# Kernel tuning notes

Hardware: AMD Instinct MI355X
Metric: run time of the kernel (lower is better)

Reference implementation:

```python
import jax, jax.numpy as jnp
import numpy as np

DIM = 192
NH = 4
B, H, W = 4, 128, 128


def _conv1x1(x, w, b):
    # x: [b,c,h,w], w: [o,c], b: [o]
    return jnp.einsum('oc,bchw->bohw', w, x) + b[None, :, None, None]


def _dwconv3(x, w, b):
    # depthwise 3x3, w: [C,1,3,3]
    y = jax.lax.conv_general_dilated(
        x, w, window_strides=(1, 1), padding='SAME',
        feature_group_count=x.shape[1],
        dimension_numbers=('NCHW', 'OIHW', 'NCHW'))
    return y + b[None, :, None, None]


def _to_heads(x, nh):
    b, c, h, w = x.shape
    return x.reshape(b, nh, c // nh, h * w)  # b head c (hw)


def _l2norm(x):
    # torch F.normalize(dim=-1): x / max(||x||, eps)
    n = jnp.sqrt(jnp.sum(x * x, axis=-1, keepdims=True))
    return x / jnp.maximum(n, 1e-12)


def _chan_attn(q, k, v, temp):
    # q,k,v: [b,head,c,n]; temp: [head,1,1] -> broadcasts over [b,head,c,c]
    scores = jnp.einsum('bhcn,bhdn->bhcd', q, k) * temp
    a = jax.nn.softmax(scores, axis=-1)
    return jnp.einsum('bhcd,bhdn->bhcn', a, v)


def setup_inputs() -> dict:
    key = jax.random.key(0)
    ks = jax.random.split(key, 16)
    d3 = 3 * DIM
    inp = {
        'sar': jax.random.normal(ks[0], (B, DIM, H, W), jnp.float32),
        'ms': jax.random.normal(ks[1], (B, DIM, H, W), jnp.float32),
        'ms_qkv_w': jax.random.normal(ks[2], (d3, DIM), jnp.float32) * 0.02,
        'ms_qkv_b': jnp.zeros((d3,), jnp.float32),
        'ms_dw_w': jax.random.normal(ks[3], (d3, 1, 3, 3), jnp.float32) * 0.1,
        'ms_dw_b': jnp.zeros((d3,), jnp.float32),
        'ms_temp': jnp.ones((NH, 1, 1), jnp.float32),
        'sar_qkv_w': jax.random.normal(ks[4], (d3, DIM), jnp.float32) * 0.02,
        'sar_qkv_b': jnp.zeros((d3,), jnp.float32),
        'sar_dw_w': jax.random.normal(ks[5], (d3, 1, 3, 3), jnp.float32) * 0.1,
        'sar_dw_b': jnp.zeros((d3,), jnp.float32),
        'sar_temp': jnp.ones((NH, 1, 1), jnp.float32),
        'ms_proj_w': jax.random.normal(ks[6], (DIM, 2 * DIM), jnp.float32) * 0.02,
        'ms_proj_b': jnp.zeros((DIM,), jnp.float32),
        'sar_proj_w': jax.random.normal(ks[7], (DIM, DIM), jnp.float32) * 0.02,
        'sar_proj_b': jnp.zeros((DIM,), jnp.float32),
    }
    return inp


def reference(sar, ms, ms_qkv_w, ms_qkv_b, ms_dw_w, ms_dw_b, ms_temp,
              sar_qkv_w, sar_qkv_b, sar_dw_w, sar_dw_b, sar_temp,
              ms_proj_w, ms_proj_b, sar_proj_w, sar_proj_b):
    b, c, h, w = ms.shape

    ms_qkv = _dwconv3(_conv1x1(ms, ms_qkv_w, ms_qkv_b), ms_dw_w, ms_dw_b)
    ms_q, ms_k, ms_v = jnp.split(ms_qkv, 3, axis=1)
    ms_q = _l2norm(_to_heads(ms_q, NH))
    ms_k = _l2norm(_to_heads(ms_k, NH))
    ms_v = _to_heads(ms_v, NH)

    sar_qkv = _dwconv3(_conv1x1(sar, sar_qkv_w, sar_qkv_b), sar_dw_w, sar_dw_b)
    sar_q, sar_k, sar_v = jnp.split(sar_qkv, 3, axis=1)
    sar_q = _l2norm(_to_heads(sar_q, NH))
    sar_k = _l2norm(_to_heads(sar_k, NH))
    sar_v = _to_heads(sar_v, NH)

    ms_self = _chan_attn(ms_q, ms_k, ms_v, ms_temp).reshape(b, c, h, w)
    sar_self = _chan_attn(sar_q, sar_k, sar_v, sar_temp).reshape(b, c, h, w)
    cross = _chan_attn(sar_q, ms_k, sar_v, ms_temp).reshape(b, c, h, w)

    sar_out = sar + _conv1x1(sar_self, sar_proj_w, sar_proj_b)
    ms_cat = jnp.concatenate([ms_self, cross + ms_self], axis=1)
    ms_out = ms + _conv1x1(ms_cat, ms_proj_w, ms_proj_b)
    return (sar_out, ms_out)
```

## Files before the change

kernel.cpp:

```cpp
#include <hip/hip_runtime.h>
#include <hip/hip_bf16.h>
#include <cstdint>

#define DIMC 192
#define BB 4
#define NN 16384
#define D3 576
#define CHD 48
#define WWID 128
#define HHGT 128
#define NCK 64
#define CKW 256

typedef short short8 __attribute__((ext_vector_type(8)));
typedef float f32x4 __attribute__((ext_vector_type(4)));

union FragU { uint4 u4; short8 s8; };

__device__ __forceinline__ float bf2f(uint16_t v) {
    return __uint_as_float(((uint32_t)v) << 16);
}
__device__ __forceinline__ float2 upk2(uint32_t u) {
    float2 r;
    r.x = __uint_as_float(u << 16);
    r.y = __uint_as_float(u & 0xffff0000u);
    return r;
}
__device__ __forceinline__ uint16_t f2bf(float f) {
    uint32_t x = __float_as_uint(f);
    return (uint16_t)((x + 0x7fffu + ((x >> 16) & 1u)) >> 16);
}
__device__ __forceinline__ uint4 pack8(const uint16_t* v) {
    uint4 u;
    u.x = (uint32_t)v[0] | ((uint32_t)v[1] << 16);
    u.y = (uint32_t)v[2] | ((uint32_t)v[3] << 16);
    u.z = (uint32_t)v[4] | ((uint32_t)v[5] << 16);
    u.w = (uint32_t)v[6] | ((uint32_t)v[7] << 16);
    return u;
}

__global__ __launch_bounds__(256) void k_prep(
    const float* __restrict__ w0, const float* __restrict__ w1,
    const float* __restrict__ w2, const float* __restrict__ w3,
    uint16_t* __restrict__ o0, uint16_t* __restrict__ o1,
    uint16_t* __restrict__ o2a, uint16_t* __restrict__ o2b,
    uint16_t* __restrict__ o3)
{
    int i = blockIdx.x * 256 + threadIdx.x;
    if (i < 110592) { o0[i] = f2bf(w0[i]); return; }
    i -= 110592;
    if (i < 110592) { o1[i] = f2bf(w1[i]); return; }
    i -= 110592;
    if (i < 36864) {
        const int o = i / DIMC, c = i % DIMC;
        o2a[i] = f2bf(w2[o * 384 + c] + w2[o * 384 + DIMC + c]);
        o2b[i] = f2bf(w2[o * 384 + DIMC + c]);
        return;
    }
    i -= 36864;
    if (i < 36864) o3[i] = f2bf(w3[i]);
}

__global__ __launch_bounds__(512, 4) void k_conv_both(
    const float* __restrict__ ms, const float* __restrict__ sarp,
    const uint16_t* __restrict__ w_ms, const uint16_t* __restrict__ w_sar,
    const float* __restrict__ b_ms, const float* __restrict__ b_sar,
    uint16_t* __restrict__ out_ms, uint16_t* __restrict__ out_sar)
{
    __shared__ uint16_t xs[128][200];
    __shared__ uint16_t wstA[64][200];
    const int t = threadIdx.x;
    const int bid = blockIdx.x;
    const int path = bid >> 9;
    const int rem = bid & 511;
    const int nb = rem & 127, b = rem >> 7;
    const int n0 = nb * 128;

    const float* x        = path ? sarp  : ms;
    const uint16_t* wsrc  = path ? w_sar : w_ms;
    const float* bias     = path ? b_sar : b_ms;
    uint16_t* out         = path ? out_sar : out_ms;

    const int lane = t & 63, wvid = t >> 6;
    const int lm = lane & 15, g = lane >> 4;
    const int wm = wvid >> 2, wn = wvid & 3;
    const int wm_ = t >> 3, wq = t & 7;

    {
        const int sn = t & 127, kq = t >> 7;
        const int sg = (sn >> 3) & 3;
        const float* xcol = x + ((size_t)b * DIMC + kq * 48) * NN + n0 + sn;
        for (int u = 0; u < 6; ++u) {
            uint16_t vals[8];
#pragma unroll
            for (int j = 0; j < 8; ++j)
                vals[j] = f2bf(xcol[(size_t)(u * 8 + j) * NN]);
            *(uint4*)&xs[sn][((kq * 6 + u) ^ sg) * 8] = pack8(vals);
        }
    }
    {
        const uint16_t* wrow = wsrc + (size_t)wm_ * DIMC;
#pragma unroll
        for (int i = 0; i < 3; ++i) {
            const int unit = i * 8 + wq;
            *(uint4*)&wstA[wm_][(unit ^ (wm_ & 7)) * 8] = *(const uint4*)&wrow[unit * 8];
        }
    }
    __syncthreads();

    FragU bfr[6][2];
#pragma unroll
    for (int ks = 0; ks < 6; ++ks)
#pragma unroll
        for (int nj = 0; nj < 2; ++nj) {
            const int row = wn * 32 + nj * 16 + lm;
            bfr[ks][nj].u4 = *(const uint4*)&xs[row][((ks * 4 + g) ^ ((row >> 3) & 3)) * 8];
        }
    __syncthreads();

    uint16_t* xsf  = &xs[0][0];
    uint16_t* wstB = xsf;
    uint16_t* sw   = xsf + 12800 + wvid * 1280;

    for (int mb = 0; mb < 9; ++mb) {
        const uint16_t* cur = (mb & 1) ? wstB : &wstA[0][0];
        uint16_t* nxt       = (mb & 1) ? &wstA[0][0] : wstB;
        uint4 wreg[3];
        if (mb < 8) {
            const uint16_t* wrow = wsrc + (size_t)((mb + 1) * 64 + wm_) * DIMC;
#pragma unroll
            for (int i = 0; i < 3; ++i)
                wreg[i] = *(const uint4*)&wrow[(i * 8 + wq) * 8];
        }
        f32x4 acc[2][2];
#pragma unroll
        for (int mi = 0; mi < 2; ++mi)
#pragma unroll
            for (int nj = 0; nj < 2; ++nj) acc[mi][nj] = (f32x4){0.f, 0.f, 0.f, 0.f};
#pragma unroll
        for (int ks = 0; ks < 6; ++ks) {
            FragU afr[2];
#pragma unroll
            for (int mi = 0; mi < 2; ++mi) {
                const int row = wm * 32 + mi * 16 + lm;
                afr[mi].u4 = *(const uint4*)&cur[row * 200 + ((ks * 4 + g) ^ (row & 7)) * 8];
            }
#pragma unroll
            for (int mi = 0; mi < 2; ++mi)
#pragma unroll
                for (int nj = 0; nj < 2; ++nj)
                    acc[mi][nj] = __builtin_amdgcn_mfma_f32_16x16x32_bf16(
                        afr[mi].s8, bfr[ks][nj].s8, acc[mi][nj], 0, 0, 0);
        }
        if (mb < 8) {
#pragma unroll
            for (int i = 0; i < 3; ++i) {
                const int unit = i * 8 + wq;
                *(uint4*)&nxt[wm_ * 200 + ((unit ^ (wm_ & 7))) * 8] = wreg[i];
            }
        }
#pragma unroll
        for (int mi = 0; mi < 2; ++mi) {
            const int rbase = mb * 64 + wm * 32 + mi * 16 + g * 4;
            const float4 bv = *(const float4*)&bias[rbase];
            const float bva[4] = {bv.x, bv.y, bv.z, bv.w};
#pragma unroll
            for (int nj = 0; nj < 2; ++nj)
#pragma unroll
                for (int r = 0; r < 4; ++r)
                    sw[(mi * 16 + g * 4 + r) * 40 + nj * 16 + lm] =
                        f2bf(acc[mi][nj][r] + bva[r]);
        }
        {
            const int row2 = lane >> 1, q = lane & 1;
            uint4 v0 = *(const uint4*)&sw[row2 * 40 + q * 16];
            uint4 v1 = *(const uint4*)&sw[row2 * 40 + q * 16 + 8];
            const int grow = mb * 64 + wm * 32 + row2;
            uint16_t* ob = &out[((size_t)b * D3 + grow) * NN + n0 + wn * 32 + q * 16];
            *(uint4*)ob       = v0;
            *(uint4*)(ob + 8) = v1;
        }
        __syncthreads();
    }
}

__global__ __launch_bounds__(512, 4) void k_proj_both(
    const uint16_t* __restrict__ sar_self, const uint16_t* __restrict__ ms_self,
    const uint16_t* __restrict__ crossb,
    const uint16_t* __restrict__ wp_sar, const uint16_t* __restrict__ wp1_ms,
    const uint16_t* __restrict__ wp2_ms,
    const float* __restrict__ b_sar, const float* __restrict__ b_ms,
    const float* __restrict__ resid_sar, const float* __restrict__ resid_ms,
    float* __restrict__ out_sar, float* __restrict__ out_ms)
{
    __shared__ uint16_t xs[128][200];
    __shared__ uint16_t wstA[64][200];
    const int t = threadIdx.x;
    const int bid = blockIdx.x;
    const int path = bid >> 9;
    const int rem = bid & 511;
    const int nb = rem & 127, b = rem >> 7;
    const int n0 = nb * 128;
    const int nph = path ? 2 : 1;

    const float* bias  = path ? b_ms : b_sar;
    const float* resid = path ? resid_ms : resid_sar;
    float* out         = path ? out_ms : out_sar;

    const int lane = t & 63, wvid = t >> 6;
    const int lm = lane & 15, g = lane >> 4;
    const int wm = wvid >> 2, wn = wvid & 3;
    const int wm_ = t >> 3, wq = t & 7;

    uint16_t* xsf  = &xs[0][0];
    uint16_t* wstB = xsf;

    f32x4 acc[3][2][2];
#pragma unroll
    for (int mb = 0; mb < 3; ++mb)
#pragma unroll
        for (int mi = 0; mi < 2; ++mi)
#pragma unroll
            for (int nj = 0; nj < 2; ++nj) acc[mb][mi][nj] = (f32x4){0.f, 0.f, 0.f, 0.f};

    for (int ph = 0; ph < nph; ++ph) {
        const uint16_t* xsrc = path ? (ph ? crossb : ms_self) : sar_self;
        const uint16_t* wsrc = path ? (ph ? wp2_ms : wp1_ms) : wp_sar;
        {
            const int p = t & 63, kg = t >> 6;
            const int sg = (p >> 2) & 3;
            const uint16_t* xcol = xsrc + ((size_t)b * DIMC + kg * 24) * NN + n0 + p * 2;
            for (int chn = 0; chn < 3; ++chn) {
                uint32_t v[8];
#pragma unroll
                for (int j = 0; j < 8; ++j)
                    v[j] = *(const uint32_t*)&xcol[(size_t)(chn * 8 + j) * NN];
                uint4 lo4, hi4;
                lo4.x = (v[0] & 0xffffu) | (v[1] << 16);
                lo4.y = (v[2] & 0xffffu) | (v[3] << 16);
                lo4.z = (v[4] & 0xffffu) | (v[5] << 16);
                lo4.w = (v[6] & 0xffffu) | (v[7] << 16);
                hi4.x = (v[0] >> 16) | (v[1] & 0xffff0000u);
                hi4.y = (v[2] >> 16) | (v[3] & 0xffff0000u);
                hi4.z = (v[4] >> 16) | (v[5] & 0xffff0000u);
                hi4.w = (v[6] >> 16) | (v[7] & 0xffff0000u);
                const int unit = (kg * 3 + chn) ^ sg;
                *(uint4*)&xs[p * 2][unit * 8]     = lo4;
                *(uint4*)&xs[p * 2 + 1][unit * 8] = hi4;
            }
        }
        {
            const uint16_t* wrow = wsrc + (size_t)wm_ * DIMC;
#pragma unroll
            for (int i = 0; i < 3; ++i) {
                const int unit = i * 8 + wq;
                *(uint4*)&wstA[wm_][(unit ^ (wm_ & 7)) * 8] = *(const uint4*)&wrow[unit * 8];
            }
        }
        __syncthreads();
        FragU bfr[6][2];
#pragma unroll
        for (int ks = 0; ks < 6; ++ks)
#pragma unroll
            for (int nj = 0; nj < 2; ++nj) {
                const int row = wn * 32 + nj * 16 + lm;
                bfr[ks][nj].u4 = *(const uint4*)&xs[row][((ks * 4 + g) ^ ((row >> 3) & 3)) * 8];
            }
        __syncthreads();

        for (int mb = 0; mb < 3; ++mb) {
            const uint16_t* cur = (mb & 1) ? wstB : &wstA[0][0];
            uint16_t* nxt       = (mb & 1) ? &wstA[0][0] : wstB;
            uint4 wreg[3];
            if (mb < 2) {
                const uint16_t* wrow = wsrc + (size_t)((mb + 1) * 64 + wm_) * DIMC;
#pragma unroll
                for (int i = 0; i < 3; ++i)
                    wreg[i] = *(const uint4*)&wrow[(i * 8 + wq) * 8];
            }
#pragma unroll
            for (int ks = 0; ks < 6; ++ks) {
                FragU afr[2];
#pragma unroll
                for (int mi = 0; mi < 2; ++mi) {
                    const int row = wm * 32 + mi * 16 + lm;
                    afr[mi].u4 = *(const uint4*)&cur[row * 200 + ((ks * 4 + g) ^ (row & 7)) * 8];
                }
#pragma unroll
                for (int mi = 0; mi < 2; ++mi)
#pragma unroll
                    for (int nj = 0; nj < 2; ++nj)
                        acc[mb][mi][nj] = __builtin_amdgcn_mfma_f32_16x16x32_bf16(
                            afr[mi].s8, bfr[ks][nj].s8, acc[mb][mi][nj], 0, 0, 0);
            }
            if (mb < 2) {
#pragma unroll
                for (int i = 0; i < 3; ++i) {
                    const int unit = i * 8 + wq;
                    *(uint4*)&nxt[wm_ * 200 + ((unit ^ (wm_ & 7))) * 8] = wreg[i];
                }
            }
            __syncthreads();
        }
    }
#pragma unroll
    for (int mb = 0; mb < 3; ++mb)
#pragma unroll
        for (int mi = 0; mi < 2; ++mi) {
            const int rbase = mb * 64 + wm * 32 + mi * 16 + g * 4;
            const float4 bv = *(const float4*)&bias[rbase];
            const float bva[4] = {bv.x, bv.y, bv.z, bv.w};
#pragma unroll
            for (int nj = 0; nj < 2; ++nj) {
                const int gcol = n0 + wn * 32 + nj * 16 + lm;
#pragma unroll
                for (int r = 0; r < 4; ++r) {
                    const size_t idx = ((size_t)b * DIMC + rbase + r) * NN + gcol;
                    out[idx] = resid[idx] + acc[mb][mi][nj][r] + bva[r];
                }
            }
        }
}

__global__ __launch_bounds__(256) void k_dw_both(
    const uint16_t* __restrict__ in0, const uint16_t* __restrict__ in1,
    const float* __restrict__ w_ms, const float* __restrict__ w_sar,
    const float* __restrict__ b_ms, const float* __restrict__ b_sar,
    uint16_t* __restrict__ out0, uint16_t* __restrict__ out1)
{
    __shared__ uint16_t lds[34 * 136];
    const int t = threadIdx.x;
    const int bid = blockIdx.x;
    const int yb = bid & 3;
    int bc = bid >> 2;
    const int path = (bc >= BB * D3);
    if (path) bc -= BB * D3;
    const int ch = bc % D3;
    const uint16_t* in = path ? in1 : in0;
    const float* w9    = path ? w_sar : w_ms;
    const float* bias  = path ? b_sar : b_ms;
    uint16_t* out      = path ? out1 : out0;

    const int y0 = yb * 32;
    const uint16_t* p = in + (size_t)bc * NN;

#pragma unroll
    for (int it = 0; it < 3; ++it) {
        const int u = it * 256 + t;
        if (u < 34 * 16) {
            const int r = u >> 4, seg = u & 15;
            const int gy = y0 - 1 + r;
            uint4 v = (gy >= 0 && gy < HHGT)
                ? *(const uint4*)(p + gy * WWID + seg * 8)
                : (uint4){0u, 0u, 0u, 0u};
            *(uint4*)&lds[r * 136 + seg * 8] = v;
        }
    }
    float wv[9];
#pragma unroll
    for (int k = 0; k < 9; ++k) wv[k] = w9[ch * 9 + k];
    const float base = bias[ch];
    __syncthreads();

    const int lr = t >> 3;
    const int x0 = (t & 7) * 16;
    float rv[3][18];
#pragma unroll
    for (int dy = 0; dy < 3; ++dy) {
        const uint16_t* lp = &lds[(lr + dy) * 136 + x0];
        uint4 a = *(const uint4*)lp;
        uint4 bq = *(const uint4*)(lp + 8);
        const uint16_t* av = (const uint16_t*)&a;
        const uint16_t* bv2 = (const uint16_t*)&bq;
#pragma unroll
        for (int j = 0; j < 8; ++j) {
            rv[dy][1 + j] = bf2f(av[j]);
            rv[dy][9 + j] = bf2f(bv2[j]);
        }
        rv[dy][0]  = (x0 > 0) ? bf2f(lds[(lr + dy) * 136 + x0 - 1]) : 0.f;
        rv[dy][17] = (x0 + 16 < WWID) ? bf2f(lds[(lr + dy) * 136 + x0 + 16]) : 0.f;
    }
    uint16_t ov[16];
#pragma unroll
    for (int j = 0; j < 16; ++j) {
        float a = base;
#pragma unroll
        for (int dy = 0; dy < 3; ++dy)
            a = fmaf(rv[dy][j], wv[dy * 3],
                fmaf(rv[dy][j + 1], wv[dy * 3 + 1],
                fmaf(rv[dy][j + 2], wv[dy * 3 + 2], a)));
        ov[j] = f2bf(a);
    }
    uint16_t* ob = out + (size_t)bc * NN + (y0 + lr) * WWID + x0;
    *(uint4*)ob       = pack8(&ov[0]);
    *(uint4*)(ob + 8) = pack8(&ov[8]);
}

__global__ __launch_bounds__(256) void k_scores_mfma(
    const uint16_t* __restrict__ qkv_ms, const uint16_t* __restrict__ qkv_sar,
    float* __restrict__ partial, float* __restrict__ sumsq)
{
    const int t = threadIdx.x;
    const int bid = blockIdx.x;
    const int ck = bid & (NCK - 1);
    const int pid = bid / NCK;
    const int h = pid & 3, b = pid >> 2;
    const int n0 = ck * CKW;
    const int lane = t & 63, w = t >> 6;

    const uint16_t* qm  = qkv_ms  + ((size_t)b * D3 + h * CHD) * NN;
    const uint16_t* km  = qkv_ms  + ((size_t)b * D3 + DIMC + h * CHD) * NN;
    const uint16_t* qsr = qkv_sar + ((size_t)b * D3 + h * CHD) * NN;
    const uint16_t* ksr = qkv_sar + ((size_t)b * D3 + DIMC + h * CHD) * NN;

    if (w < 3) {
        const uint16_t* qb = (w == 0) ? qm : qsr;
        const uint16_t* kb = (w == 1) ? ksr : km;
        const int lm = lane & 15, g = lane >> 4;
        f32x4 acc[3][3];
#pragma unroll
        for (int i = 0; i < 3; ++i)
#pragma unroll
            for (int j = 0; j < 3; ++j) acc[i][j] = (f32x4){0.f, 0.f, 0.f, 0.f};
#pragma unroll 2
        for (int kk = 0; kk < CKW / 32; ++kk) {
            const int nb2 = n0 + kk * 32 + g * 8;
            FragU qf[3], kf[3];
#pragma unroll
            for (int i = 0; i < 3; ++i)
                qf[i].u4 = *(const uint4*)&qb[(size_t)(i * 16 + lm) * NN + nb2];
#pragma unroll
            for (int j = 0; j < 3; ++j)
                kf[j].u4 = *(const uint4*)&kb[(size_t)(j * 16 + lm) * NN + nb2];
#pragma unroll
            for (int i = 0; i < 3; ++i)
#pragma unroll
                for (int j = 0; j < 3; ++j)
                    acc[i][j] = __builtin_amdgcn_mfma_f32_16x16x32_bf16(
                        qf[i].s8, kf[j].s8, acc[i][j], 0, 0, 0);
        }
        float* pd = partial + (((size_t)pid * 3 + w) * NCK + ck) * 2304;
        const int g4 = g * 4;
#pragma unroll
        for (int i = 0; i < 3; ++i)
#pragma unroll
            for (int j = 0; j < 3; ++j)
#pragma unroll
                for (int r = 0; r < 4; ++r)
                    pd[(i * 16 + g4 + r) * 48 + j * 16 + lm] = acc[i][j][r];
    } else {
#pragma unroll
        for (int rep = 0; rep < 3; ++rep) {
            const int rid = rep * 64 + lane;
            const int s = rid / CHD, c = rid % CHD;
            const uint16_t* rowp =
                (s == 0) ? qm  + (size_t)c * NN :
                (s == 1) ? km  + (size_t)c * NN :
                (s == 2) ? qsr + (size_t)c * NN :
                           ksr + (size_t)c * NN;
            float sum = 0.f;
#pragma unroll 4
            for (int u = 0; u < CKW / 8; ++u) {
                uint4 v = *(const uint4*)&rowp[n0 + u * 8];
                uint32_t uu[4] = {v.x, v.y, v.z, v.w};
#pragma unroll
                for (int q = 0; q < 4; ++q) {
                    float2 f = upk2(uu[q]);
                    sum = fmaf(f.x, f.x, fmaf(f.y, f.y, sum));
                }
            }
            sumsq[(((size_t)pid * NCK + ck) * 4 + s) * CHD + c] = sum;
        }
    }
}

__global__ __launch_bounds__(64) void k_softmax(
    const float* __restrict__ partial, const float* __restrict__ sumsq,
    const float* __restrict__ ms_temp, const float* __restrict__ sar_temp,
    float* __restrict__ A)
{
    const int lane = threadIdx.x;
    const int bi = blockIdx.x;
    const int c = bi % 48;
    const int pid = bi / 48;
    const int h = pid & 3, b = (pid >> 2) & 3, type = pid >> 4;
    const int pid16 = b * 4 + h;
    float s;
    if (lane < 48) {
        float accv = 0.f;
        const float* pp = partial + ((size_t)pid16 * 3 + type) * NCK * 2304 + c * 48 + lane;
#pragma unroll 8
        for (int ck = 0; ck < NCK; ++ck) accv += pp[(size_t)ck * 2304];
        const int qset = (type == 0) ? 0 : 2;
        const int kset = (type == 1) ? 3 : 1;
        float qsum = 0.f, ksum = 0.f;
        const float* sq = sumsq + (size_t)pid16 * NCK * 4 * CHD;
#pragma unroll 8
        for (int ck = 0; ck < NCK; ++ck) {
            qsum += sq[ck * 4 * CHD + qset * CHD + c];
            ksum += sq[ck * 4 * CHD + kset * CHD + lane];
        }
        const float tval = (type == 1) ? sar_temp[h] : ms_temp[h];
        const float qsc = 1.0f / fmaxf(sqrtf(qsum), 1e-12f);
        const float ksc = 1.0f / fmaxf(sqrtf(ksum), 1e-12f);
        s = accv * qsc * ksc * tval;
    } else {
        s = -3.0e38f;
    }
    float m = s;
#pragma unroll
    for (int o = 32; o > 0; o >>= 1) m = fmaxf(m, __shfl_xor(m, o));
    float e = (lane < 48) ? __expf(s - m) : 0.f;
    float sum = e;
#pragma unroll
    for (int o = 32; o > 0; o >>= 1) sum += __shfl_xor(sum, o);
    if (lane < 48) A[(size_t)pid * 2304 + c * 48 + lane] = e / sum;
}

__global__ __launch_bounds__(256) void k_apply_mfma(
    const float* __restrict__ A, const uint16_t* __restrict__ qkv_ms,
    const uint16_t* __restrict__ qkv_sar, uint16_t* __restrict__ attn)
{
    __shared__ uint16_t vs[256][40];
    __shared__ uint16_t as[48][40];
    __shared__ uint16_t sw_all[4][48][72];
    const int t = threadIdx.x;
    const int nb = blockIdx.x & 63;
    const int pid = blockIdx.x >> 6;
    const int h = pid & 3, b = (pid >> 2) & 3, type = pid >> 4;
    const int n0 = nb * 256;
    const uint16_t* vsrc = (type == 0) ? qkv_ms : qkv_sar;
    const uint16_t* vb = vsrc + ((size_t)b * D3 + 2 * DIMC + (size_t)h * CHD) * NN;
    const float* Ap = A + (size_t)pid * 2304;

    const int lane = t & 63, wvid = t >> 6;
    const int lm = lane & 15, g = lane >> 4;

    f32x4 acc[3][4];
#pragma unroll
    for (int i = 0; i < 3; ++i)
#pragma unroll
        for (int j = 0; j < 4; ++j) acc[i][j] = (f32x4){0.f, 0.f, 0.f, 0.f};

    for (int k0 = 0; k0 < 64; k0 += 32) {
        __syncthreads();
#pragma unroll
        for (int kh = 0; kh < 2; ++kh) {
            uint16_t vals[16];
#pragma unroll
            for (int j = 0; j < 16; ++j) {
                const int d = k0 + kh * 16 + j;
                vals[j] = (d < CHD) ? vb[(size_t)d * NN + n0 + t] : (uint16_t)0;
            }
            const int u0 = (2 * kh) ^ ((t >> 3) & 3);
            const int u1 = (2 * kh + 1) ^ ((t >> 3) & 3);
            *(uint4*)&vs[t][u0 * 8] = pack8(&vals[0]);
            *(uint4*)&vs[t][u1 * 8] = pack8(&vals[8]);
        }
        if (t < 192) {
            const int c = t >> 2, dq = t & 3;
            uint16_t av[8];
#pragma unroll
            for (int i = 0; i < 8; ++i) {
                const int d = k0 + dq * 8 + i;
                av[i] = (d < CHD) ? f2bf(Ap[c * CHD + d]) : (uint16_t)0;
            }
            const int u = dq ^ ((c >> 3) & 3);
            *(uint4*)&as[c][u * 8] = pack8(av);
        }
        __syncthreads();
        FragU afr[3], bfr[4];
#pragma unroll
        for (int mi = 0; mi < 3; ++mi) {
            const int row = mi * 16 + lm;
            afr[mi].u4 = *(const uint4*)&as[row][(g ^ ((row >> 3) & 3)) * 8];
        }
#pragma unroll
        for (int nj = 0; nj < 4; ++nj) {
            const int row = wvid * 64 + nj * 16 + lm;
            bfr[nj].u4 = *(const uint4*)&vs[row][(g ^ ((row >> 3) & 3)) * 8];
        }
#pragma unroll
        for (int mi = 0; mi < 3; ++mi)
#pragma unroll
            for (int nj = 0; nj < 4; ++nj)
                acc[mi][nj] = __builtin_amdgcn_mfma_f32_16x16x32_bf16(
                    afr[mi].s8, bfr[nj].s8, acc[mi][nj], 0, 0, 0);
    }

    uint16_t* ob = attn + (size_t)type * BB * DIMC * NN +
                   ((size_t)b * DIMC + (size_t)h * CHD) * NN;
    uint16_t* sw = &sw_all[wvid][0][0];
#pragma unroll
    for (int mi = 0; mi < 3; ++mi)
#pragma unroll
        for (int nj = 0; nj < 4; ++nj)
#pragma unroll
            for (int r = 0; r < 4; ++r)
                sw[(mi * 16 + g * 4 + r) * 72 + nj * 16 + lm] = f2bf(acc[mi][nj][r]);
    const int l8 = lane & 7, r8 = lane >> 3;
#pragma unroll
    for (int pass = 0; pass < 6; ++pass) {
        const int rr = pass * 8 + r8;
        uint4 v = *(const uint4*)&sw[rr * 72 + l8 * 8];
        *(uint4*)&ob[(size_t)rr * NN + n0 + wvid * 64 + l8 * 8] = v;
    }
}

extern "C" void kernel_launch(void* const* d_in, const int* in_sizes, int n_in,
                              void* d_out, int out_size, void* d_ws, size_t ws_size,
                              hipStream_t stream)
{
    const float* sar        = (const float*)d_in[0];
    const float* ms         = (const float*)d_in[1];
    const float* ms_qkv_w   = (const float*)d_in[2];
    const float* ms_qkv_b   = (const float*)d_in[3];
    const float* ms_dw_w    = (const float*)d_in[4];
    const float* ms_dw_b    = (const float*)d_in[5];
    const float* ms_temp    = (const float*)d_in[6];
    const float* sar_qkv_w  = (const float*)d_in[7];
    const float* sar_qkv_b  = (const float*)d_in[8];
    const float* sar_dw_w   = (const float*)d_in[9];
    const float* sar_dw_b   = (const float*)d_in[10];
    const float* sar_temp   = (const float*)d_in[11];
    const float* ms_proj_w  = (const float*)d_in[12];
    const float* ms_proj_b  = (const float*)d_in[13];
    const float* sar_proj_w = (const float*)d_in[14];
    const float* sar_proj_b = (const float*)d_in[15];

    char* ws = (char*)d_ws;
    uint16_t* tmp     = (uint16_t*)(ws);
    uint16_t* tmp2    = (uint16_t*)(d_out);
    uint16_t* qkv_ms  = (uint16_t*)(ws + 75497472ull);
    uint16_t* qkv_sar = (uint16_t*)(ws + 150994944ull);
    float* partial    = (float*)(ws);
    float* sumsq      = (float*)(ws + 33554432ull);
    float* Amat       = (float*)(ws + 230043648ull);
    uint16_t* wq_ms   = (uint16_t*)(ws + 230486016ull);
    uint16_t* wq_sar  = (uint16_t*)(ws + 230707200ull);
    uint16_t* wp1_ms  = (uint16_t*)(ws + 230928384ull);
    uint16_t* wp2_ms  = (uint16_t*)(ws + 231002112ull);
    uint16_t* wp_sar  = (uint16_t*)(ws + 231075840ull);
    uint16_t* attn    = tmp;

    float* out_sar = (float*)d_out;
    float* out_ms  = out_sar + (size_t)BB * DIMC * NN;

    dim3 b256(256);
    k_prep<<<dim3(1152), b256, 0, stream>>>(ms_qkv_w, sar_qkv_w, ms_proj_w, sar_proj_w,
                                            wq_ms, wq_sar, wp1_ms, wp2_ms, wp_sar);
    k_conv_both<<<dim3(1024), dim3(512), 0, stream>>>(
        ms, sar, wq_ms, wq_sar, ms_qkv_b, sar_qkv_b, tmp, tmp2);
    k_dw_both<<<dim3(2 * BB * D3 * 4), b256, 0, stream>>>(
        tmp, tmp2, ms_dw_w, sar_dw_w, ms_dw_b, sar_dw_b, qkv_ms, qkv_sar);

    k_scores_mfma<<<dim3(16 * NCK), b256, 0, stream>>>(qkv_ms, qkv_sar, partial, sumsq);
    k_softmax<<<dim3(48 * 48), dim3(64), 0, stream>>>(partial, sumsq, ms_temp, sar_temp, Amat);
    k_apply_mfma<<<dim3(48 * 64), b256, 0, stream>>>(Amat, qkv_ms, qkv_sar, attn);

    uint16_t* ms_self  = attn;
    uint16_t* sar_self = attn + (size_t)BB * DIMC * NN;
    uint16_t* crossb   = attn + 2ull * BB * DIMC * NN;
    k_proj_both<<<dim3(1024), dim3(512), 0, stream>>>(
        sar_self, ms_self, crossb, wp_sar, wp1_ms, wp2_ms,
        sar_proj_b, ms_proj_b, sar, ms, out_sar, out_ms);
}
```

Before: 324.4 us.

## Halve pixel tile and block size in 1x1 conv and projection kernels

The qkv conv and output projection kernels now process 64-pixel tiles with 256-thread blocks instead of 128-pixel tiles with 512 threads, doubling the grid to 2048 blocks. The LDS XOR swizzles are removed in favour of plain row-major indexing, and in the conv kernel the double-buffered weight staging becomes a single buffer reloaded after an extra barrier. The aim is more, smaller blocks with less shared memory each, for better occupancy and load balance. The cost is more redundant weight loads per pixel, possible LDS bank conflicts without the swizzle, and an added sync per weight tile.

```diff
diff --git a/kernel.cpp b/kernel.cpp
--- a/kernel.cpp
+++ b/kernel.cpp
@@ -61,20 +61,20 @@
     if (i < 36864) o3[i] = f2bf(w3[i]);
 }
 
-__global__ __launch_bounds__(512, 4) void k_conv_both(
+__global__ __launch_bounds__(256, 3) void k_conv_both(
     const float* __restrict__ ms, const float* __restrict__ sarp,
     const uint16_t* __restrict__ w_ms, const uint16_t* __restrict__ w_sar,
     const float* __restrict__ b_ms, const float* __restrict__ b_sar,
     uint16_t* __restrict__ out_ms, uint16_t* __restrict__ out_sar)
 {
-    __shared__ uint16_t xs[128][200];
-    __shared__ uint16_t wstA[64][200];
+    __shared__ uint16_t xs[64][200];
+    __shared__ uint16_t wst[64][200];
     const int t = threadIdx.x;
     const int bid = blockIdx.x;
-    const int path = bid >> 9;
-    const int rem = bid & 511;
-    const int nb = rem & 127, b = rem >> 7;
-    const int n0 = nb * 128;
+    const int path = bid >> 10;
+    const int rem = bid & 1023;
+    const int nb = rem & 255, b = rem >> 8;
+    const int n0 = nb * 64;
 
     const float* x        = path ? sarp  : ms;
     const uint16_t* wsrc  = path ? w_sar : w_ms;
@@ -83,27 +83,26 @@
 
     const int lane = t & 63, wvid = t >> 6;
     const int lm = lane & 15, g = lane >> 4;
-    const int wm = wvid >> 2, wn = wvid & 3;
-    const int wm_ = t >> 3, wq = t & 7;
+    const int wm = wvid >> 1, wn = wvid & 1;
+    const int wm_ = t >> 2, wq = t & 3;
 
     {
-        const int sn = t & 127, kq = t >> 7;
-        const int sg = (sn >> 3) & 3;
-        const float* xcol = x + ((size_t)b * DIMC + kq * 48) * NN + n0 + sn;
+        const int sn = t & 63, kh = t >> 6;
+        const float* xcol = x + ((size_t)b * DIMC + kh * 48) * NN + n0 + sn;
         for (int u = 0; u < 6; ++u) {
             uint16_t vals[8];
 #pragma unroll
             for (int j = 0; j < 8; ++j)
                 vals[j] = f2bf(xcol[(size_t)(u * 8 + j) * NN]);
-            *(uint4*)&xs[sn][((kq * 6 + u) ^ sg) * 8] = pack8(vals);
+            *(uint4*)&xs[sn][(kh * 6 + u) * 8] = pack8(vals);
         }
     }
     {
         const uint16_t* wrow = wsrc + (size_t)wm_ * DIMC;
 #pragma unroll
-        for (int i = 0; i < 3; ++i) {
-            const int unit = i * 8 + wq;
-            *(uint4*)&wstA[wm_][(unit ^ (wm_ & 7)) * 8] = *(const uint4*)&wrow[unit * 8];
+        for (int i = 0; i < 6; ++i) {
+            const int unit = i * 4 + wq;
+            *(uint4*)&wst[wm_][unit * 8] = *(const uint4*)&wrow[unit * 8];
         }
     }
     __syncthreads();
@@ -114,23 +113,19 @@
 #pragma unroll
         for (int nj = 0; nj < 2; ++nj) {
             const int row = wn * 32 + nj * 16 + lm;
-            bfr[ks][nj].u4 = *(const uint4*)&xs[row][((ks * 4 + g) ^ ((row >> 3) & 3)) * 8];
+            bfr[ks][nj].u4 = *(const uint4*)&xs[row][ks * 32 + g * 8];
         }
     __syncthreads();
 
-    uint16_t* xsf  = &xs[0][0];
-    uint16_t* wstB = xsf;
-    uint16_t* sw   = xsf + 12800 + wvid * 1280;
+    uint16_t* sw = &xs[0][0] + wvid * 1280;
 
     for (int mb = 0; mb < 9; ++mb) {
-        const uint16_t* cur = (mb & 1) ? wstB : &wstA[0][0];
-        uint16_t* nxt       = (mb & 1) ? &wstA[0][0] : wstB;
-        uint4 wreg[3];
+        uint4 wreg[6];
         if (mb < 8) {
             const uint16_t* wrow = wsrc + (size_t)((mb + 1) * 64 + wm_) * DIMC;
 #pragma unroll
-            for (int i = 0; i < 3; ++i)
-                wreg[i] = *(const uint4*)&wrow[(i * 8 + wq) * 8];
+            for (int i = 0; i < 6; ++i)
+                wreg[i] = *(const uint4*)&wrow[(i * 4 + wq) * 8];
         }
         f32x4 acc[2][2];
 #pragma unroll
@@ -143,7 +138,7 @@
 #pragma unroll
             for (int mi = 0; mi < 2; ++mi) {
                 const int row = wm * 32 + mi * 16 + lm;
-                afr[mi].u4 = *(const uint4*)&cur[row * 200 + ((ks * 4 + g) ^ (row & 7)) * 8];
+                afr[mi].u4 = *(const uint4*)&wst[row][ks * 32 + g * 8];
             }
 #pragma unroll
             for (int mi = 0; mi < 2; ++mi)
@@ -151,13 +146,6 @@
                 for (int nj = 0; nj < 2; ++nj)
                     acc[mi][nj] = __builtin_amdgcn_mfma_f32_16x16x32_bf16(
                         afr[mi].s8, bfr[ks][nj].s8, acc[mi][nj], 0, 0, 0);
-        }
-        if (mb < 8) {
-#pragma unroll
-            for (int i = 0; i < 3; ++i) {
-                const int unit = i * 8 + wq;
-                *(uint4*)&nxt[wm_ * 200 + ((unit ^ (wm_ & 7))) * 8] = wreg[i];
-            }
         }
 #pragma unroll
         for (int mi = 0; mi < 2; ++mi) {
@@ -172,19 +160,28 @@
                         f2bf(acc[mi][nj][r] + bva[r]);
         }
         {
-            const int row2 = lane >> 1, q = lane & 1;
-            uint4 v0 = *(const uint4*)&sw[row2 * 40 + q * 16];
-            uint4 v1 = *(const uint4*)&sw[row2 * 40 + q * 16 + 8];
-            const int grow = mb * 64 + wm * 32 + row2;
-            uint16_t* ob = &out[((size_t)b * D3 + grow) * NN + n0 + wn * 32 + q * 16];
-            *(uint4*)ob       = v0;
-            *(uint4*)(ob + 8) = v1;
+            const int c8 = (lane & 3) * 8;
+#pragma unroll
+            for (int pass = 0; pass < 2; ++pass) {
+                const int r2 = pass * 16 + (lane >> 2);
+                uint4 v = *(const uint4*)&sw[r2 * 40 + c8];
+                const int grow = mb * 64 + wm * 32 + r2;
+                *(uint4*)&out[((size_t)b * D3 + grow) * NN + n0 + wn * 32 + c8] = v;
+            }
         }
         __syncthreads();
-    }
-}
-
-__global__ __launch_bounds__(512, 4) void k_proj_both(
+        if (mb < 8) {
+#pragma unroll
+            for (int i = 0; i < 6; ++i) {
+                const int unit = i * 4 + wq;
+                *(uint4*)&wst[wm_][unit * 8] = wreg[i];
+            }
+            __syncthreads();
+        }
+    }
+}
+
+__global__ __launch_bounds__(256, 3) void k_proj_both(
     const uint16_t* __restrict__ sar_self, const uint16_t* __restrict__ ms_self,
     const uint16_t* __restrict__ crossb,
     const uint16_t* __restrict__ wp_sar, const uint16_t* __restrict__ wp1_ms,
@@ -193,14 +190,14 @@
     const float* __restrict__ resid_sar, const float* __restrict__ resid_ms,
     float* __restrict__ out_sar, float* __restrict__ out_ms)
 {
-    __shared__ uint16_t xs[128][200];
+    __shared__ uint16_t xs[64][200];
     __shared__ uint16_t wstA[64][200];
     const int t = threadIdx.x;
     const int bid = blockIdx.x;
-    const int path = bid >> 9;
-    const int rem = bid & 511;
-    const int nb = rem & 127, b = rem >> 7;
-    const int n0 = nb * 128;
+    const int path = bid >> 10;
+    const int rem = bid & 1023;
+    const int nb = rem & 255, b = rem >> 8;
+    const int n0 = nb * 64;
     const int nph = path ? 2 : 1;
 
     const float* bias  = path ? b_ms : b_sar;
@@ -209,8 +206,8 @@
 
     const int lane = t & 63, wvid = t >> 6;
     const int lm = lane & 15, g = lane >> 4;
-    const int wm = wvid >> 2, wn = wvid & 3;
-    const int wm_ = t >> 3, wq = t & 7;
+    const int wm = wvid >> 1, wn = wvid & 1;
+    const int wm_ = t >> 2, wq = t & 3;
 
     uint16_t* xsf  = &xs[0][0];
     uint16_t* wstB = xsf;
@@ -227,8 +224,7 @@
         const uint16_t* xsrc = path ? (ph ? crossb : ms_self) : sar_self;
         const uint16_t* wsrc = path ? (ph ? wp2_ms : wp1_ms) : wp_sar;
         {
-            const int p = t & 63, kg = t >> 6;
-            const int sg = (p >> 2) & 3;
+            const int p = t & 31, kg = t >> 5;
             const uint16_t* xcol = xsrc + ((size_t)b * DIMC + kg * 24) * NN + n0 + p * 2;
             for (int chn = 0; chn < 3; ++chn) {
                 uint32_t v[8];
@@ -244,7 +240,7 @@
                 hi4.y = (v[2] >> 16) | (v[3] & 0xffff0000u);
                 hi4.z = (v[4] >> 16) | (v[5] & 0xffff0000u);
                 hi4.w = (v[6] >> 16) | (v[7] & 0xffff0000u);
-                const int unit = (kg * 3 + chn) ^ sg;
+                const int unit = kg * 3 + chn;
                 *(uint4*)&xs[p * 2][unit * 8]     = lo4;
                 *(uint4*)&xs[p * 2 + 1][unit * 8] = hi4;
             }
@@ -252,9 +248,9 @@
         {
             const uint16_t* wrow = wsrc + (size_t)wm_ * DIMC;
 #pragma unroll
-            for (int i = 0; i < 3; ++i) {
-                const int unit = i * 8 + wq;
-                *(uint4*)&wstA[wm_][(unit ^ (wm_ & 7)) * 8] = *(const uint4*)&wrow[unit * 8];
+            for (int i = 0; i < 6; ++i) {
+                const int unit = i * 4 + wq;
+                *(uint4*)&wstA[wm_][unit * 8] = *(const uint4*)&wrow[unit * 8];
             }
         }
         __syncthreads();
@@ -264,19 +260,19 @@
 #pragma unroll
             for (int nj = 0; nj < 2; ++nj) {
                 const int row = wn * 32 + nj * 16 + lm;
-                bfr[ks][nj].u4 = *(const uint4*)&xs[row][((ks * 4 + g) ^ ((row >> 3) & 3)) * 8];
+                bfr[ks][nj].u4 = *(const uint4*)&xs[row][ks * 32 + g * 8];
             }
         __syncthreads();
 
         for (int mb = 0; mb < 3; ++mb) {
             const uint16_t* cur = (mb & 1) ? wstB : &wstA[0][0];
             uint16_t* nxt       = (mb & 1) ? &wstA[0][0] : wstB;
-            uint4 wreg[3];
+            uint4 wreg[6];
             if (mb < 2) {
                 const uint16_t* wrow = wsrc + (size_t)((mb + 1) * 64 + wm_) * DIMC;
 #pragma unroll
-                for (int i = 0; i < 3; ++i)
-                    wreg[i] = *(const uint4*)&wrow[(i * 8 + wq) * 8];
+                for (int i = 0; i < 6; ++i)
+                    wreg[i] = *(const uint4*)&wrow[(i * 4 + wq) * 8];
             }
 #pragma unroll
             for (int ks = 0; ks < 6; ++ks) {
@@ -284,7 +280,7 @@
 #pragma unroll
                 for (int mi = 0; mi < 2; ++mi) {
                     const int row = wm * 32 + mi * 16 + lm;
-                    afr[mi].u4 = *(const uint4*)&cur[row * 200 + ((ks * 4 + g) ^ (row & 7)) * 8];
+                    afr[mi].u4 = *(const uint4*)&cur[row * 200 + ks * 32 + g * 8];
                 }
 #pragma unroll
                 for (int mi = 0; mi < 2; ++mi)
@@ -295,9 +291,9 @@
             }
             if (mb < 2) {
 #pragma unroll
-                for (int i = 0; i < 3; ++i) {
-                    const int unit = i * 8 + wq;
-                    *(uint4*)&nxt[wm_ * 200 + ((unit ^ (wm_ & 7))) * 8] = wreg[i];
+                for (int i = 0; i < 6; ++i) {
+                    const int unit = i * 4 + wq;
+                    *(uint4*)&nxt[wm_ * 200 + unit * 8] = wreg[i];
                 }
             }
             __syncthreads();
@@ -649,7 +645,7 @@
     dim3 b256(256);
     k_prep<<<dim3(1152), b256, 0, stream>>>(ms_qkv_w, sar_qkv_w, ms_proj_w, sar_proj_w,
                                             wq_ms, wq_sar, wp1_ms, wp2_ms, wp_sar);
-    k_conv_both<<<dim3(1024), dim3(512), 0, stream>>>(
+    k_conv_both<<<dim3(2048), b256, 0, stream>>>(
         ms, sar, wq_ms, wq_sar, ms_qkv_b, sar_qkv_b, tmp, tmp2);
     k_dw_both<<<dim3(2 * BB * D3 * 4), b256, 0, stream>>>(
         tmp, tmp2, ms_dw_w, sar_dw_w, ms_dw_b, sar_dw_b, qkv_ms, qkv_sar);
@@ -661,7 +657,7 @@
     uint16_t* ms_self  = attn;
     uint16_t* sar_self = attn + (size_t)BB * DIMC * NN;
     uint16_t* crossb   = attn + 2ull * BB * DIMC * NN;
-    k_proj_both<<<dim3(1024), dim3(512), 0, stream>>>(
+    k_proj_both<<<dim3(2048), b256, 0, stream>>>(
         sar_self, ms_self, crossb, wp_sar, wp1_ms, wp2_ms,
         sar_proj_b, ms_proj_b, sar, ms, out_sar, out_ms);
 }
```

New measurement: 408.6 us. 26.0% more time.
